# Kernel optimization log

Hardware: AMD Instinct MI355X
Metric: run time of the kernel (lower is better)

The kernel has to match this reference:

```python
import jax, jax.numpy as jnp
import numpy as np

B, I, C, H, QP, VP = 2, 1024, 16, 12, 4, 8
W_C = (2.0 / (9.0 * QP)) ** 0.5
W_L = (1.0 / 3.0) ** 0.5


def setup_inputs() -> dict:
    key = jax.random.key(0)
    ks = jax.random.split(key, 14)
    rn = lambda k, shape, s=1.0: (jax.random.normal(k, shape, dtype=jnp.float32) * s)
    return {
        "s": rn(ks[0], (B, I, C)),
        "z": rn(ks[1], (B, I, I, C)),
        "R": rn(ks[2], (B, I, 3, 3)),
        "t": rn(ks[3], (B, I, 3)),
        "Wq": rn(ks[4], (C, C * H), C ** -0.5),
        "Wk": rn(ks[5], (C, C * H), C ** -0.5),
        "Wv": rn(ks[6], (C, C * H), C ** -0.5),
        "Wb": rn(ks[7], (C, H), C ** -0.5),
        "Wqp": rn(ks[8], (C, 3 * QP * H), C ** -0.5),
        "Wkp": rn(ks[9], (C, 3 * QP * H), C ** -0.5),
        "Wvp": rn(ks[10], (C, 3 * VP * H), C ** -0.5),
        "gamma": rn(ks[11], (H,), 0.5),
        "Wout": rn(ks[12], (H * (2 * C + 4 * VP), C), (H * (2 * C + 4 * VP)) ** -0.5),
        "bout": rn(ks[13], (C,), 0.02),
    }


def _apply_rigid(R, t, p):
    # p: (B, i, n, 3); rigid transform per residue: R @ p + t
    return jnp.einsum("bixy,bipy->bipx", R, p) + t[:, :, None, :]


def reference(s, z, R, t, Wq, Wk, Wv, Wb, Wqp, Wkp, Wvp, gamma, Wout, bout):
    b_, i_, c = s.shape
    h, qp, vp = gamma.shape[0], Wqp.shape[1] // (3 * gamma.shape[0]), Wvp.shape[1] // (3 * gamma.shape[0])

    q = (s @ Wq).reshape(b_, i_, h, c)
    k = (s @ Wk).reshape(b_, i_, h, c)
    v = (s @ Wv).reshape(b_, i_, h, c)

    q_pts = _apply_rigid(R, t, (s @ Wqp).reshape(b_, i_, h * qp, 3)).reshape(b_, i_, h, qp, 3)
    k_pts = _apply_rigid(R, t, (s @ Wkp).reshape(b_, i_, h * qp, 3)).reshape(b_, i_, h, qp, 3)
    v_pts = _apply_rigid(R, t, (s @ Wvp).reshape(b_, i_, h * vp, 3)).reshape(b_, i_, h, vp, 3)

    bias = jnp.einsum("bijc,ch->bhij", z, Wb)
    a = jnp.einsum("bihc,bjhc->bhij", q, k) * (c ** -0.5) + bias

    # squared point distances summed over points, expanded to avoid (B,i,j,h,P,3) tensor
    q2 = jnp.sum(q_pts ** 2, axis=(-1, -2))          # (B,i,h)
    k2 = jnp.sum(k_pts ** 2, axis=(-1, -2))          # (B,j,h)
    qk = jnp.einsum("bihpx,bjhpx->bhij", q_pts, k_pts)
    d2 = q2.transpose(0, 2, 1)[..., None] + k2.transpose(0, 2, 1)[:, :, None, :] - 2.0 * qk  # (B,h,i,j)

    head_w = jax.nn.softplus(gamma)                  # (h,)
    a = a + d2 * (head_w[None, :, None, None] * W_C * -0.5)
    a = a * W_L
    a = jax.nn.softmax(a, axis=-2)  # NOTE: original code softmaxes over dim=-2 (the i axis)

    # NOTE: original einsum indexes v by i (not j); replicated faithfully
    o = jnp.einsum("bhij,bihc->bihc", a, v).reshape(b_, i_, h * c)

    o_pts = jnp.einsum("bhij,bjhpx->bihpx", a, v_pts)  # (B,i,h,vp,3)
    o_pts_norm = jnp.sqrt(jnp.maximum(jnp.sum(o_pts ** 2, axis=-1), 1e-12)).reshape(b_, i_, h * vp)
    o_pts_flat = o_pts.reshape(b_, i_, h * vp * 3)

    o_pair = jnp.einsum("bhij,bijc->bihc", a, z).reshape(b_, i_, h * c)

    cat = jnp.concatenate([o, o_pair, o_pts_flat, o_pts_norm], axis=-1)
    return cat @ Wout + bout
```

## Files before the change

### kernel.cpp

```cpp
#include <hip/hip_runtime.h>
#include <hip/hip_bf16.h>
#include <math.h>

#define B_ 2
#define I_ 1024
#define C_ 16
#define H_ 12

__device__ __constant__ float kW_C = 0.23570226039551584f;
#define W_Lc 0.5773502691896258f
#define LOG2E 1.4426950408889634f

typedef _Float16 hf;
typedef hf hf2 __attribute__((ext_vector_type(2)));
typedef hf hf4v __attribute__((ext_vector_type(4)));
typedef hf hf8v __attribute__((ext_vector_type(8)));
typedef float f32x4 __attribute__((ext_vector_type(4)));
typedef unsigned int u32;

template <typename T, typename F>
__device__ inline T bc(F f) { return __builtin_bit_cast(T, f); }

__device__ inline float fdot2f(u32 a, u32 b, float c) {
#if __has_builtin(__builtin_amdgcn_fdot2)
  return __builtin_amdgcn_fdot2(bc<hf2>(a), bc<hf2>(b), c, false);
#else
  hf2 x = bc<hf2>(a), y = bc<hf2>(b);
  return c + (float)x[0] * (float)y[0] + (float)x[1] * (float)y[1];
#endif
}

__device__ inline u32 pkrtz(float lo, float hi) {
#if __has_builtin(__builtin_amdgcn_cvt_pkrtz)
  return bc<u32>(__builtin_amdgcn_cvt_pkrtz(lo, hi));
#else
  hf2 t; t[0] = (hf)lo; t[1] = (hf)hi; return bc<u32>(t);
#endif
}

__device__ inline u32 permlo(u32 hiw, u32 low) {
#if __has_builtin(__builtin_amdgcn_perm)
  return __builtin_amdgcn_perm(hiw, low, 0x05040100u);
#else
  return (low & 0xffffu) | (hiw << 16);
#endif
}
__device__ inline u32 permhi(u32 hiw, u32 low) {
#if __has_builtin(__builtin_amdgcn_perm)
  return __builtin_amdgcn_perm(hiw, low, 0x07060302u);
#else
  return (low >> 16) | (hiw & 0xffff0000u);
#endif
}

#define QF16_OFF 0
#define QF16_SZ (B_*I_*196)
#define KF16_OFF (QF16_OFF + QF16_SZ)
#define KF16_SZ QF16_SZ
#define VPF_OFF (KF16_OFF + KF16_SZ)
#define VPF_SZ (B_*I_*144)
#define VV_OFF (VPF_OFF + VPF_SZ)
#define VV_SZ (B_*I_*192)
#define SM_OFF (VV_OFF + VV_SZ)
#define SM_SZ (B_*12*1024*2)
#define PM_OFF (SM_OFF + SM_SZ)
#define PM_SZ (B_*64*32*192*2)
#define LT_OFF (PM_OFF + PM_SZ)
#define LT_SZ (B_*H_*512*1024)
#define ACC2_OFF (LT_OFF + LT_SZ)

__global__ __launch_bounds__(192) void kA(const float* __restrict__ s, const float* __restrict__ R,
                 const float* __restrict__ t, const float* __restrict__ Wq,
                 const float* __restrict__ Wk, const float* __restrict__ Wv,
                 const float* __restrict__ Wqp, const float* __restrict__ Wkp,
                 const float* __restrict__ Wvp, const float* __restrict__ gam,
                 float* __restrict__ ws) {
  int blk = blockIdx.x;
  int b = blk >> 10, i = blk & 1023;
  int tid = threadIdx.x;
  __shared__ float sl[16], rl[9], tl[3], part[96];
  if (tid < 16) sl[tid] = s[(b*I_ + i)*C_ + tid];
  else if (tid < 25) rl[tid-16] = R[(size_t)(b*I_+i)*9 + (tid-16)];
  else if (tid < 28) tl[tid-25] = t[(size_t)(b*I_+i)*3 + (tid-25)];
  __syncthreads();
  hf* QF  = (hf*)(ws + QF16_OFF) + (size_t)(b*I_+i)*392;
  hf* KF  = (hf*)(ws + KF16_OFF) + (size_t)(b*I_+i)*392;
  ushort* VPP = (ushort*)(ws + VPF_OFF);
  float* vv = ws + VV_OFF + (size_t)(b*I_+i)*192;
  {
    int hc = tid; int h = hc >> 4, c = hc & 15;
    float aq = 0.f, ak = 0.f, av = 0.f;
    #pragma unroll
    for (int ci = 0; ci < 16; ci++) {
      float sv = sl[ci];
      aq += sv * Wq[ci*192 + hc];
      ak += sv * Wk[ci*192 + hc];
      av += sv * Wv[ci*192 + hc];
    }
    const float s_qk = 0.25f * W_Lc * LOG2E;
    QF[h*32 + c] = (hf)(aq * s_qk);
    KF[h*32 + c] = (hf)ak;
    vv[hc] = av;
  }
  {
    float raw[3], px[3];
    if (tid < 96) {
      bool isq = tid < 48;
      int n = isq ? tid : tid - 48;
      const float* W = isq ? Wqp : Wkp;
      #pragma unroll
      for (int x = 0; x < 3; x++) {
        float a2 = 0.f;
        #pragma unroll
        for (int ci = 0; ci < 16; ci++) a2 += sl[ci] * W[ci*144 + n*3 + x];
        raw[x] = a2;
      }
      #pragma unroll
      for (int x = 0; x < 3; x++)
        px[x] = rl[x*3]*raw[0] + rl[x*3+1]*raw[1] + rl[x*3+2]*raw[2] + tl[x];
      int h = n >> 2, p = n & 3;
      part[tid] = px[0]*px[0] + px[1]*px[1] + px[2]*px[2];
      if (isq) {
        float g = gam[h];
        float sp = log1pf(expf(g));
        float coef2 = -0.5f * kW_C * sp * W_Lc * LOG2E;
        #pragma unroll
        for (int x = 0; x < 3; x++) QF[h*32 + 16 + p*3 + x] = (hf)(px[x] * (-2.0f * coef2));
      } else {
        #pragma unroll
        for (int x = 0; x < 3; x++) KF[h*32 + 16 + p*3 + x] = (hf)px[x];
      }
    } else {
      int n = tid - 96;
      #pragma unroll
      for (int x = 0; x < 3; x++) {
        float a2 = 0.f;
        #pragma unroll
        for (int ci = 0; ci < 16; ci++) a2 += sl[ci] * Wvp[ci*288 + n*3 + x];
        raw[x] = a2;
      }
      #pragma unroll
      for (int x = 0; x < 3; x++)
        px[x] = rl[x*3]*raw[0] + rl[x*3+1]*raw[1] + rl[x*3+2]*raw[2] + tl[x];
      int h = n >> 3, p = n & 7;
      size_t base = ((size_t)(b*512 + (i >> 1))*12 + h)*48 + (i & 1);
      #pragma unroll
      for (int x = 0; x < 3; x++) VPP[base + (p*3 + x)*2] = bc<ushort>((hf)px[x]);
    }
  }
  __syncthreads();
  if (tid < 24) {
    int h = tid % 12; bool isq = tid < 12;
    float g = gam[h];
    float sp = log1pf(expf(g));
    float coef2 = -0.5f * kW_C * sp * W_Lc * LOG2E;
    float s2 = 0.f;
    int base = isq ? h*4 : 48 + h*4;
    #pragma unroll
    for (int p = 0; p < 4; p++) s2 += part[base + p];
    if (isq) {
      QF[h*32 + 28] = (hf)(coef2 * s2);
      QF[h*32 + 29] = (hf)1.0f;
      QF[h*32 + 30] = (hf)0.0f;
      QF[h*32 + 31] = (hf)0.0f;
    } else {
      KF[h*32 + 28] = (hf)1.0f;
      KF[h*32 + 29] = (hf)(coef2 * s2);
      KF[h*32 + 30] = (hf)0.0f;
      KF[h*32 + 31] = (hf)0.0f;
    }
  }
}

__global__ __launch_bounds__(256,4) void kB(const float* __restrict__ z,
                 const float* __restrict__ Wb, float* __restrict__ ws) {
  int blk = blockIdx.x;
  int icb = blk & 7; int jt = (blk >> 3) & 63; int b = blk >> 9;
  int tid = threadIdx.x;
  int w = tid >> 6, lane = tid & 63;
  int ln15 = lane & 15, l16 = lane >> 4;
  int j0 = jt*16;
  int icw = icb*4 + w;
  __shared__ u32 lb[4*16*113];
  int wbase = w*(16*113);
  const ushort* QFu = (const ushort*)(ws + QF16_OFF);
  const ushort* KFu = (const ushort*)(ws + KF16_OFF);
  hf4v wbf;
  #pragma unroll
  for (int e = 0; e < 4; e++) {
    int c = l16*4 + e;
    float v = (ln15 < 12) ? Wb[c*12 + ln15] * (W_Lc*LOG2E) : 0.f;
    wbf[e] = (hf)v;
  }
  u32* LTu_w = (u32*)(ws + LT_OFF);
  float m[12], S[12];
  #pragma unroll
  for (int h = 0; h < 12; h++) { m[h] = -1e30f; S[h] = 0.f; }
  for (int tt = 0; tt < 2; ++tt) {
    int i0 = icw*32 + tt*16;
    #pragma unroll 4
    for (int ii = 0; ii < 16; ++ii) {
      float4 zv = *(const float4*)(z + ((size_t)(b*I_ + i0 + ii)*I_ + j0 + ln15)*16 + l16*4);
      uint2 ap = make_uint2(pkrtz(zv.x, zv.y), pkrtz(zv.z, zv.w));
      hf4v a = bc<hf4v>(ap);
      f32x4 cb = {0.f, 0.f, 0.f, 0.f};
      cb = __builtin_amdgcn_mfma_f32_16x16x16f16(a, wbf, cb, 0, 0, 0);
      if (ln15 < 12) {
        lb[wbase + ii*113 + ln15*9 + l16*2]     = pkrtz(cb[0], cb[1]);
        lb[wbase + ii*113 + ln15*9 + l16*2 + 1] = pkrtz(cb[2], cb[3]);
      }
    }
    #pragma unroll
    for (int h = 0; h < 12; ++h) {
      hf8v aq = *(const hf8v*)&QFu[(size_t)(b*I_ + i0 + ln15)*392 + h*32 + l16*8];
      hf8v bk = *(const hf8v*)&KFu[(size_t)(b*I_ + j0 + ln15)*392 + h*32 + l16*8];
      f32x4 c = {0.f, 0.f, 0.f, 0.f};
      c = __builtin_amdgcn_mfma_f32_16x16x32_f16(aq, bk, c, 0, 0, 0);
      int ib = wbase + (l16*4)*113 + h*9 + (ln15 >> 1);
      int par = (ln15 & 1) << 4;
      float l0 = c[0] + (float)bc<hf>((ushort)(lb[ib]       >> par));
      float l1 = c[1] + (float)bc<hf>((ushort)(lb[ib + 113] >> par));
      float l2 = c[2] + (float)bc<hf>((ushort)(lb[ib + 226] >> par));
      float l3 = c[3] + (float)bc<hf>((ushort)(lb[ib + 339] >> par));
      hf h0 = (hf)l0, h1 = (hf)l1, h2 = (hf)l2, h3 = (hf)l3;
      float r0 = (float)h0, r1 = (float)h1, r2 = (float)h2, r3 = (float)h3;
      float mx = fmaxf(fmaxf(r0, r1), fmaxf(r2, r3));
      mx = fmaxf(mx, __shfl_xor(mx, 16));
      mx = fmaxf(mx, __shfl_xor(mx, 32));
      float es = __builtin_amdgcn_exp2f(r0 - mx) + __builtin_amdgcn_exp2f(r1 - mx)
               + __builtin_amdgcn_exp2f(r2 - mx) + __builtin_amdgcn_exp2f(r3 - mx);
      es += __shfl_xor(es, 16);
      es += __shfl_xor(es, 32);
      float mn = fmaxf(m[h], mx);
      S[h] = S[h] * __builtin_amdgcn_exp2f(m[h] - mn) + es * __builtin_amdgcn_exp2f(mx - mn);
      m[h] = mn;
      u32 me01 = (u32)bc<ushort>(h0) | ((u32)bc<ushort>(h1) << 16);
      u32 me23 = (u32)bc<ushort>(h2) | ((u32)bc<ushort>(h3) << 16);
      u32 p01 = (u32)__shfl_xor((int)me01, 1);
      u32 p23 = (u32)__shfl_xor((int)me23, 1);
      if ((ln15 & 1) == 0) {
        u32 w0 = permlo(p01, me01), w1 = permhi(p01, me01);
        u32 w2 = permlo(p23, me23), w3 = permhi(p23, me23);
        u32* dst = LTu_w + ((size_t)(b*12 + h)*512 + jt*8 + (ln15 >> 1))*1024 + i0 + l16*4;
        *(uint4*)dst = make_uint4(w0, w1, w2, w3);
      }
    }
  }
  if (l16 == 0) {
    float2* pm = (float2*)(ws + PM_OFF) + ((size_t)((b*64 + jt)*32 + icw))*192;
    #pragma unroll
    for (int h = 0; h < 12; ++h) pm[h*16 + ln15] = make_float2(m[h], S[h]);
  }
}

__global__ __launch_bounds__(192) void kB2(float* __restrict__ ws) {
  int blk = blockIdx.x; int jt = blk & 63, b = blk >> 6;
  int tid = threadIdx.x; int h = tid >> 4, jl = tid & 15;
  const float2* pm = (const float2*)(ws + PM_OFF) + (size_t)(b*64+jt)*32*192 + tid;
  float m = -1e30f, S = 0.f;
  #pragma unroll
  for (int ic = 0; ic < 32; ic++) {
    float2 p = pm[ic*192];
    float mn = fmaxf(m, p.x);
    S = S * __builtin_amdgcn_exp2f(m - mn) + p.y * __builtin_amdgcn_exp2f(p.x - mn);
    m = mn;
  }
  int j = jt*16 + jl;
  float* sm = ws + SM_OFF + ((size_t)((b*12+h)*1024) + j)*2;
  sm[0] = m;
  sm[1] = 1.0f / S;
}

__global__ __launch_bounds__(192,6) void kC(const float* __restrict__ z,
                 float* __restrict__ ws, int jsh) {
  int blk = blockIdx.x;
  int jch = 1 << jsh;
  int jc = blk & (jch-1); int it = (blk >> jsh) & 63; int b = blk >> (jsh+6);
  int tid = threadIdx.x; int h = tid >> 4, il = tid & 15;
  int i = it*16 + il;
  __shared__ u32 llds[96*18];
  __shared__ u32 zplds[16*132];
  float opts[24], opair[16], rsum = 0.f;
  #pragma unroll
  for (int n = 0; n < 24; n++) opts[n] = 0.f;
  #pragma unroll
  for (int c = 0; c < 16; c++) opair[c] = 0.f;
  const u32* LTu = (const u32*)(ws + LT_OFF);
  const float* SM = ws + SM_OFF + (size_t)((b*12+h)*1024)*2;
  const ushort* VPP = (const ushort*)(ws + VPF_OFF);
  int chunk = I_ >> jsh;
  int nt = chunk >> 4;
  int hh = tid >> 4, rr = tid & 15, sjp = rr >> 1, sq = rr & 1;
  for (int t = 0; t < nt; ++t) {
    int j0 = jc*chunk + t*16;
    int jpg0 = j0 >> 1;
    __syncthreads();
    {
      const u32* src = LTu + ((size_t)(b*12+hh)*512 + jpg0 + sjp)*1024 + it*16 + sq*8;
      uint4 a = *(const uint4*)src;
      uint4 c4 = *(const uint4*)(src + 4);
      u32* drow = llds + (hh*8 + sjp)*18 + sq*8;
      *(uint2*)(drow + 0) = make_uint2(a.x, a.y);
      *(uint2*)(drow + 2) = make_uint2(a.z, a.w);
      *(uint2*)(drow + 4) = make_uint2(c4.x, c4.y);
      *(uint2*)(drow + 6) = make_uint2(c4.z, c4.w);
    }
    for (int idx = tid; idx < 512; idx += 192) {
      int r = idx >> 5, jp = (idx >> 2) & 7, c4 = idx & 3;
      const float* zb = z + ((size_t)(b*I_ + it*16 + r)*I_ + j0 + 2*jp)*16 + c4*4;
      float4 a = *(const float4*)zb;
      float4 d = *(const float4*)(zb + 16);
      uint4 o = make_uint4(pkrtz(a.x, d.x), pkrtz(a.y, d.y), pkrtz(a.z, d.z), pkrtz(a.w, d.w));
      *(uint4*)&zplds[r*132 + jp*16 + c4*4] = o;
    }
    __syncthreads();
    #pragma unroll 1
    for (int jp = 0; jp < 8; ++jp) {
      u32 lp = llds[(h*8 + jp)*18 + il];
      float4 st = *(const float4*)(SM + (size_t)(j0 + 2*jp)*2);
      const uint4* vp4 = (const uint4*)(VPP + ((size_t)(b*512 + jpg0 + jp)*12 + h)*48);
      uint4 va = vp4[0], vb = vp4[1], vc = vp4[2];
      uint4 vd = vp4[3], ve = vp4[4], vf = vp4[5];
      hf2 lh = bc<hf2>(lp);
      float w0 = __builtin_amdgcn_exp2f((float)lh[0] - st.x) * st.y;
      float w1 = __builtin_amdgcn_exp2f((float)lh[1] - st.z) * st.w;
      rsum += w0 + w1;
      u32 w2 = pkrtz(w0, w1);
      const u32* zr = &zplds[il*132 + jp*16];
      uint4 p0 = *(const uint4*)(zr + 0), p1 = *(const uint4*)(zr + 4);
      uint4 p2 = *(const uint4*)(zr + 8), p3 = *(const uint4*)(zr + 12);
      opair[0]  = fdot2f(w2, p0.x, opair[0]);
      opair[1]  = fdot2f(w2, p0.y, opair[1]);
      opair[2]  = fdot2f(w2, p0.z, opair[2]);
      opair[3]  = fdot2f(w2, p0.w, opair[3]);
      opair[4]  = fdot2f(w2, p1.x, opair[4]);
      opair[5]  = fdot2f(w2, p1.y, opair[5]);
      opair[6]  = fdot2f(w2, p1.z, opair[6]);
      opair[7]  = fdot2f(w2, p1.w, opair[7]);
      opair[8]  = fdot2f(w2, p2.x, opair[8]);
      opair[9]  = fdot2f(w2, p2.y, opair[9]);
      opair[10] = fdot2f(w2, p2.z, opair[10]);
      opair[11] = fdot2f(w2, p2.w, opair[11]);
      opair[12] = fdot2f(w2, p3.x, opair[12]);
      opair[13] = fdot2f(w2, p3.y, opair[13]);
      opair[14] = fdot2f(w2, p3.z, opair[14]);
      opair[15] = fdot2f(w2, p3.w, opair[15]);
      opts[0]  = fdot2f(w2, va.x, opts[0]);
      opts[1]  = fdot2f(w2, va.y, opts[1]);
      opts[2]  = fdot2f(w2, va.z, opts[2]);
      opts[3]  = fdot2f(w2, va.w, opts[3]);
      opts[4]  = fdot2f(w2, vb.x, opts[4]);
      opts[5]  = fdot2f(w2, vb.y, opts[5]);
      opts[6]  = fdot2f(w2, vb.z, opts[6]);
      opts[7]  = fdot2f(w2, vb.w, opts[7]);
      opts[8]  = fdot2f(w2, vc.x, opts[8]);
      opts[9]  = fdot2f(w2, vc.y, opts[9]);
      opts[10] = fdot2f(w2, vc.z, opts[10]);
      opts[11] = fdot2f(w2, vc.w, opts[11]);
      opts[12] = fdot2f(w2, vd.x, opts[12]);
      opts[13] = fdot2f(w2, vd.y, opts[13]);
      opts[14] = fdot2f(w2, vd.z, opts[14]);
      opts[15] = fdot2f(w2, vd.w, opts[15]);
      opts[16] = fdot2f(w2, ve.x, opts[16]);
      opts[17] = fdot2f(w2, ve.y, opts[17]);
      opts[18] = fdot2f(w2, ve.z, opts[18]);
      opts[19] = fdot2f(w2, ve.w, opts[19]);
      opts[20] = fdot2f(w2, vf.x, opts[20]);
      opts[21] = fdot2f(w2, vf.y, opts[21]);
      opts[22] = fdot2f(w2, vf.z, opts[22]);
      opts[23] = fdot2f(w2, vf.w, opts[23]);
    }
  }
  ushort* ab = (ushort*)(ws + ACC2_OFF) + ((size_t)(b*I_+i)*jch + jc)*512;
  #pragma unroll
  for (int n = 0; n < 24; n++) ab[h*24 + n] = bc<ushort>((hf)opts[n]);
  #pragma unroll
  for (int c = 0; c < 16; c++) ab[288 + h*16 + c] = bc<ushort>((hf)opair[c]);
  ab[480 + h] = bc<ushort>((hf)rsum);
}

__global__ __launch_bounds__(256) void kD(const float* __restrict__ Wout, const float* __restrict__ bout,
                 const float* __restrict__ ws, float* __restrict__ out, int jsh) {
  int jch = 1 << jsh;
  int blk = blockIdx.x;
  int b = blk >> 8; int i0 = (blk & 255) << 2;
  int tid = threadIdx.x;
  __shared__ float accs[4*512];
  __shared__ float cat[4*776];
  __shared__ float red[256];
  const ushort* ACC2us = (const ushort*)(ws + ACC2_OFF);
  for (int idx = tid; idx < 4*512; idx += 256) {
    int r = idx >> 9, f = idx & 511;
    const ushort* src = ACC2us + (size_t)(b*I_+i0+r)*jch*512 + f;
    float ssum = 0.f;
    for (int jc = 0; jc < jch; jc++) ssum += (float)bc<hf>(src[jc*512]);
    accs[idx] = ssum;
  }
  __syncthreads();
  const float* vv = ws + VV_OFF;
  for (int idx = tid; idx < 4*768; idx += 256) {
    int r = idx / 768, f = idx - r*768;
    int i = i0 + r;
    const float* ab = accs + r*512;
    float val;
    if (f < 192) {
      int h = f >> 4, c = f & 15;
      val = vv[(size_t)(b*I_+i)*192 + h*16 + c] * ab[480 + h];
    } else if (f < 384) {
      val = ab[288 + (f - 192)];
    } else if (f < 672) {
      val = ab[f - 384];
    } else {
      int g = f - 672; int base = (g >> 3)*24 + (g & 7)*3;
      float x0 = ab[base], x1 = ab[base+1], x2 = ab[base+2];
      val = sqrtf(fmaxf(x0*x0 + x1*x1 + x2*x2, 1e-12f));
    }
    cat[r*776 + f] = val;
  }
  __syncthreads();
  {
    int r = tid >> 6, c = (tid >> 2) & 15, sseg = tid & 3;
    const float* cr = cat + r*776;
    float a = 0.f;
    for (int f = sseg*192; f < sseg*192 + 192; f++) a += cr[f] * Wout[f*16 + c];
    red[tid] = a;
  }
  __syncthreads();
  if ((tid & 3) == 0) {
    int r = tid >> 6, c = (tid >> 2) & 15;
    float sum = bout[c] + red[tid] + red[tid+1] + red[tid+2] + red[tid+3];
    out[((size_t)(b*I_) + i0 + r)*16 + c] = sum;
  }
}

extern "C" void kernel_launch(void* const* d_in, const int* in_sizes, int n_in,
                              void* d_out, int out_size, void* d_ws, size_t ws_size,
                              hipStream_t stream) {
  const float* s    = (const float*)d_in[0];
  const float* z    = (const float*)d_in[1];
  const float* R    = (const float*)d_in[2];
  const float* t    = (const float*)d_in[3];
  const float* Wq   = (const float*)d_in[4];
  const float* Wk   = (const float*)d_in[5];
  const float* Wv   = (const float*)d_in[6];
  const float* Wb   = (const float*)d_in[7];
  const float* Wqp  = (const float*)d_in[8];
  const float* Wkp  = (const float*)d_in[9];
  const float* Wvp  = (const float*)d_in[10];
  const float* gam  = (const float*)d_in[11];
  const float* Wout = (const float*)d_in[12];
  const float* bout = (const float*)d_in[13];
  float* out = (float*)d_out;
  float* ws = (float*)d_ws;

  int jsh = 4;
  while (jsh > 0) {
    size_t need = ((size_t)ACC2_OFF + (size_t)B_*I_*(1u<<jsh)*256) * 4u;
    if (need <= ws_size) break;
    jsh--;
  }

  hipLaunchKernelGGL(kA, dim3(B_*I_), dim3(192), 0, stream,
                     s, R, t, Wq, Wk, Wv, Wqp, Wkp, Wvp, gam, ws);
  hipLaunchKernelGGL(kB, dim3(B_*64*8), dim3(256), 0, stream, z, Wb, ws);
  hipLaunchKernelGGL(kB2, dim3(B_*64), dim3(192), 0, stream, ws);
  hipLaunchKernelGGL(kC, dim3(B_*64*(1<<jsh)), dim3(192), 0, stream, z, ws, jsh);
  hipLaunchKernelGGL(kD, dim3(B_*256), dim3(256), 0, stream, Wout, bout, ws, out, jsh);
}
```

Measured before the change: 177.2 us.

## Split kB into smaller blocks with batched z loads and prefetched Q/K features

kB now uses 128-thread blocks, each wave handling 16 i-rows instead of 32, and the grid grows fourfold. Each wave emits per-16-row partial (max, sum) softmax statistics, so the partial buffer and the kB2 reduction double to 64 chunks. z rows are loaded eight at a time ahead of the MFMAs, and the Q/K feature loads for the next head are prefetched. The aim is more parallelism and better latency hiding for the z stream, paid for with more partial-statistic traffic and more kB2 reduction work.

Result: no change. 180.5 us (+1.9%).

```diff
diff --git a/kernel.cpp b/kernel.cpp
--- a/kernel.cpp
+++ b/kernel.cpp
@@ -64,7 +64,7 @@
 #define SM_OFF (VV_OFF + VV_SZ)
 #define SM_SZ (B_*12*1024*2)
 #define PM_OFF (SM_OFF + SM_SZ)
-#define PM_SZ (B_*64*32*192*2)
+#define PM_SZ (B_*64*64*192*2)
 #define LT_OFF (PM_OFF + PM_SZ)
 #define LT_SZ (B_*H_*512*1024)
 #define ACC2_OFF (LT_OFF + LT_SZ)
@@ -172,16 +172,17 @@
   }
 }
 
-__global__ __launch_bounds__(256,4) void kB(const float* __restrict__ z,
+__global__ __launch_bounds__(128,6) void kB(const float* __restrict__ z,
                  const float* __restrict__ Wb, float* __restrict__ ws) {
   int blk = blockIdx.x;
-  int icb = blk & 7; int jt = (blk >> 3) & 63; int b = blk >> 9;
+  int icb = blk & 31; int jt = (blk >> 5) & 63; int b = blk >> 11;
   int tid = threadIdx.x;
   int w = tid >> 6, lane = tid & 63;
   int ln15 = lane & 15, l16 = lane >> 4;
   int j0 = jt*16;
-  int icw = icb*4 + w;
-  __shared__ u32 lb[4*16*113];
+  int icw = icb*2 + w;
+  int i0 = icw*16;
+  __shared__ u32 lb[2*16*113];
   int wbase = w*(16*113);
   const ushort* QFu = (const ushort*)(ws + QF16_OFF);
   const ushort* KFu = (const ushort*)(ws + KF16_OFF);
@@ -193,14 +194,25 @@
     wbf[e] = (hf)v;
   }
   u32* LTu_w = (u32*)(ws + LT_OFF);
-  float m[12], S[12];
-  #pragma unroll
-  for (int h = 0; h < 12; h++) { m[h] = -1e30f; S[h] = 0.f; }
-  for (int tt = 0; tt < 2; ++tt) {
-    int i0 = icw*32 + tt*16;
-    #pragma unroll 4
-    for (int ii = 0; ii < 16; ++ii) {
-      float4 zv = *(const float4*)(z + ((size_t)(b*I_ + i0 + ii)*I_ + j0 + ln15)*16 + l16*4);
+  #pragma unroll
+  for (int bat = 0; bat < 2; ++bat) {
+    float4 zr0, zr1, zr2, zr3, zr4, zr5, zr6, zr7;
+    {
+      const float* zb = z + ((size_t)(b*I_ + i0 + bat*8)*I_ + j0 + ln15)*16 + l16*4;
+      const size_t rs = (size_t)I_*16;
+      zr0 = *(const float4*)(zb);
+      zr1 = *(const float4*)(zb + rs);
+      zr2 = *(const float4*)(zb + rs*2);
+      zr3 = *(const float4*)(zb + rs*3);
+      zr4 = *(const float4*)(zb + rs*4);
+      zr5 = *(const float4*)(zb + rs*5);
+      zr6 = *(const float4*)(zb + rs*6);
+      zr7 = *(const float4*)(zb + rs*7);
+    }
+    #pragma unroll
+    for (int u = 0; u < 8; ++u) {
+      float4 zv = (u==0)?zr0:(u==1)?zr1:(u==2)?zr2:(u==3)?zr3:(u==4)?zr4:(u==5)?zr5:(u==6)?zr6:zr7;
+      int ii = bat*8 + u;
       uint2 ap = make_uint2(pkrtz(zv.x, zv.y), pkrtz(zv.z, zv.w));
       hf4v a = bc<hf4v>(ap);
       f32x4 cb = {0.f, 0.f, 0.f, 0.f};
@@ -210,56 +222,57 @@
         lb[wbase + ii*113 + ln15*9 + l16*2 + 1] = pkrtz(cb[2], cb[3]);
       }
     }
-    #pragma unroll
-    for (int h = 0; h < 12; ++h) {
-      hf8v aq = *(const hf8v*)&QFu[(size_t)(b*I_ + i0 + ln15)*392 + h*32 + l16*8];
-      hf8v bk = *(const hf8v*)&KFu[(size_t)(b*I_ + j0 + ln15)*392 + h*32 + l16*8];
-      f32x4 c = {0.f, 0.f, 0.f, 0.f};
-      c = __builtin_amdgcn_mfma_f32_16x16x32_f16(aq, bk, c, 0, 0, 0);
-      int ib = wbase + (l16*4)*113 + h*9 + (ln15 >> 1);
-      int par = (ln15 & 1) << 4;
-      float l0 = c[0] + (float)bc<hf>((ushort)(lb[ib]       >> par));
-      float l1 = c[1] + (float)bc<hf>((ushort)(lb[ib + 113] >> par));
-      float l2 = c[2] + (float)bc<hf>((ushort)(lb[ib + 226] >> par));
-      float l3 = c[3] + (float)bc<hf>((ushort)(lb[ib + 339] >> par));
-      hf h0 = (hf)l0, h1 = (hf)l1, h2 = (hf)l2, h3 = (hf)l3;
-      float r0 = (float)h0, r1 = (float)h1, r2 = (float)h2, r3 = (float)h3;
-      float mx = fmaxf(fmaxf(r0, r1), fmaxf(r2, r3));
-      mx = fmaxf(mx, __shfl_xor(mx, 16));
-      mx = fmaxf(mx, __shfl_xor(mx, 32));
-      float es = __builtin_amdgcn_exp2f(r0 - mx) + __builtin_amdgcn_exp2f(r1 - mx)
-               + __builtin_amdgcn_exp2f(r2 - mx) + __builtin_amdgcn_exp2f(r3 - mx);
-      es += __shfl_xor(es, 16);
-      es += __shfl_xor(es, 32);
-      float mn = fmaxf(m[h], mx);
-      S[h] = S[h] * __builtin_amdgcn_exp2f(m[h] - mn) + es * __builtin_amdgcn_exp2f(mx - mn);
-      m[h] = mn;
-      u32 me01 = (u32)bc<ushort>(h0) | ((u32)bc<ushort>(h1) << 16);
-      u32 me23 = (u32)bc<ushort>(h2) | ((u32)bc<ushort>(h3) << 16);
-      u32 p01 = (u32)__shfl_xor((int)me01, 1);
-      u32 p23 = (u32)__shfl_xor((int)me23, 1);
-      if ((ln15 & 1) == 0) {
-        u32 w0 = permlo(p01, me01), w1 = permhi(p01, me01);
-        u32 w2 = permlo(p23, me23), w3 = permhi(p23, me23);
-        u32* dst = LTu_w + ((size_t)(b*12 + h)*512 + jt*8 + (ln15 >> 1))*1024 + i0 + l16*4;
-        *(uint4*)dst = make_uint4(w0, w1, w2, w3);
-      }
-    }
-  }
-  if (l16 == 0) {
-    float2* pm = (float2*)(ws + PM_OFF) + ((size_t)((b*64 + jt)*32 + icw))*192;
-    #pragma unroll
-    for (int h = 0; h < 12; ++h) pm[h*16 + ln15] = make_float2(m[h], S[h]);
+  }
+  float2* pm = (float2*)(ws + PM_OFF) + ((size_t)((b*64 + jt)*64 + icw))*192;
+  const size_t qfb = (size_t)(b*I_ + i0 + ln15)*392 + l16*8;
+  const size_t kfb = (size_t)(b*I_ + j0 + ln15)*392 + l16*8;
+  hf8v aqn = *(const hf8v*)&QFu[qfb];
+  hf8v bkn = *(const hf8v*)&KFu[kfb];
+  #pragma unroll
+  for (int h = 0; h < 12; ++h) {
+    hf8v aq = aqn, bk = bkn;
+    if (h < 11) {
+      aqn = *(const hf8v*)&QFu[qfb + (h+1)*32];
+      bkn = *(const hf8v*)&KFu[kfb + (h+1)*32];
+    }
+    f32x4 c = {0.f, 0.f, 0.f, 0.f};
+    c = __builtin_amdgcn_mfma_f32_16x16x32_f16(aq, bk, c, 0, 0, 0);
+    int ib = wbase + (l16*4)*113 + h*9 + (ln15 >> 1);
+    int par = (ln15 & 1) << 4;
+    float l0 = c[0] + (float)bc<hf>((ushort)(lb[ib]       >> par));
+    float l1 = c[1] + (float)bc<hf>((ushort)(lb[ib + 113] >> par));
+    float l2 = c[2] + (float)bc<hf>((ushort)(lb[ib + 226] >> par));
+    float l3 = c[3] + (float)bc<hf>((ushort)(lb[ib + 339] >> par));
+    hf h0 = (hf)l0, h1 = (hf)l1, h2 = (hf)l2, h3 = (hf)l3;
+    float r0 = (float)h0, r1 = (float)h1, r2 = (float)h2, r3 = (float)h3;
+    float mx = fmaxf(fmaxf(r0, r1), fmaxf(r2, r3));
+    mx = fmaxf(mx, __shfl_xor(mx, 16));
+    mx = fmaxf(mx, __shfl_xor(mx, 32));
+    float es = __builtin_amdgcn_exp2f(r0 - mx) + __builtin_amdgcn_exp2f(r1 - mx)
+             + __builtin_amdgcn_exp2f(r2 - mx) + __builtin_amdgcn_exp2f(r3 - mx);
+    es += __shfl_xor(es, 16);
+    es += __shfl_xor(es, 32);
+    u32 me01 = (u32)bc<ushort>(h0) | ((u32)bc<ushort>(h1) << 16);
+    u32 me23 = (u32)bc<ushort>(h2) | ((u32)bc<ushort>(h3) << 16);
+    u32 p01 = (u32)__shfl_xor((int)me01, 1);
+    u32 p23 = (u32)__shfl_xor((int)me23, 1);
+    if ((ln15 & 1) == 0) {
+      u32 w0 = permlo(p01, me01), w1 = permhi(p01, me01);
+      u32 w2 = permlo(p23, me23), w3 = permhi(p23, me23);
+      u32* dst = LTu_w + ((size_t)(b*12 + h)*512 + jt*8 + (ln15 >> 1))*1024 + i0 + l16*4;
+      *(uint4*)dst = make_uint4(w0, w1, w2, w3);
+    }
+    if (l16 == 0) pm[h*16 + ln15] = make_float2(mx, es);
   }
 }
 
 __global__ __launch_bounds__(192) void kB2(float* __restrict__ ws) {
   int blk = blockIdx.x; int jt = blk & 63, b = blk >> 6;
   int tid = threadIdx.x; int h = tid >> 4, jl = tid & 15;
-  const float2* pm = (const float2*)(ws + PM_OFF) + (size_t)(b*64+jt)*32*192 + tid;
+  const float2* pm = (const float2*)(ws + PM_OFF) + (size_t)(b*64+jt)*64*192 + tid;
   float m = -1e30f, S = 0.f;
-  #pragma unroll
-  for (int ic = 0; ic < 32; ic++) {
+  #pragma unroll 4
+  for (int ic = 0; ic < 64; ic++) {
     float2 p = pm[ic*192];
     float mn = fmaxf(m, p.x);
     S = S * __builtin_amdgcn_exp2f(m - mn) + p.y * __builtin_amdgcn_exp2f(p.x - mn);
@@ -462,7 +475,7 @@
 
   hipLaunchKernelGGL(kA, dim3(B_*I_), dim3(192), 0, stream,
                      s, R, t, Wq, Wk, Wv, Wqp, Wkp, Wvp, gam, ws);
-  hipLaunchKernelGGL(kB, dim3(B_*64*8), dim3(256), 0, stream, z, Wb, ws);
+  hipLaunchKernelGGL(kB, dim3(B_*64*32), dim3(128), 0, stream, z, Wb, ws);
   hipLaunchKernelGGL(kB2, dim3(B_*64), dim3(192), 0, stream, ws);
   hipLaunchKernelGGL(kC, dim3(B_*64*(1<<jsh)), dim3(192), 0, stream, z, ws, jsh);
   hipLaunchKernelGGL(kD, dim3(B_*256), dim3(256), 0, stream, Wout, bout, ws, out, jsh);
```
